# Kernel optimization log

Hardware: AMD Instinct MI355X
Metric: run time of the kernel (lower is better)

The kernel has to match this reference:

```python
import jax, jax.numpy as jnp
import numpy as np

N_ENTITIES = 100000
N_EDGES = 600000
N_RELATIONS = 24
D = 128


def setup_inputs() -> dict:
    key = jax.random.key(0)
    k1, k2, k3, k4 = jax.random.split(key, 4)
    ego_embed = jax.random.normal(k1, (N_ENTITIES, D), dtype=jnp.float32)
    edge_index = jax.random.randint(k2, (2, N_EDGES), 0, N_ENTITIES, dtype=jnp.int64)
    edge_type = jax.random.randint(k3, (N_EDGES,), 0, N_RELATIONS, dtype=jnp.int64)
    relation_weight = jax.random.normal(k4, (N_RELATIONS, D), dtype=jnp.float32)
    return {
        "ego_embed": ego_embed,
        "edge_index": edge_index,
        "edge_type": edge_type,
        "relation_weight": relation_weight,
    }


def reference(ego_embed, edge_index, edge_type, relation_weight):
    head, tail = edge_index[0], edge_index[1]
    n_entities = ego_embed.shape[0]
    # gather tail entity embeddings and relation embeddings, form messages
    msg = ego_embed[tail] * relation_weight[edge_type]  # [E, D]
    # scatter-mean aggregate messages per head entity
    agg = jax.ops.segment_sum(msg, head, num_segments=n_entities)  # [N, D]
    cnt = jax.ops.segment_sum(
        jnp.ones((msg.shape[0], 1), dtype=msg.dtype), head, num_segments=n_entities
    )  # [N, 1]
    entity_agg = agg / jnp.maximum(cnt, jnp.asarray(1, msg.dtype))
    return entity_agg
```

## Files before the change

kernel.cpp:

```cpp
#include <hip/hip_runtime.h>

#define D 128
#define CAP 32
#define SB 512
#define NREL 24
#define ABLOCKS 2048

__device__ __forceinline__ unsigned short f2bf_rne(float f) {
    unsigned b = __float_as_uint(f);
    b += 0x7fffu + ((b >> 16) & 1u);
    return (unsigned short)(b >> 16);
}


__global__ void conv_k(const float* __restrict__ in, ushort* __restrict__ outb, int n4,
                       int* __restrict__ cnt, int nEnt) {
    int g = blockIdx.x * blockDim.x + threadIdx.x;
    int stride = gridDim.x * blockDim.x;
    for (int j = g; j < nEnt; j += stride) cnt[j] = 0;
    const float4* __restrict__ in4 = (const float4*)in;
    ushort4* __restrict__ o4 = (ushort4*)outb;
    for (int i = g; i < n4; i += stride) {
        float4 v = in4[i];
        ushort4 o;
        o.x = f2bf_rne(v.x); o.y = f2bf_rne(v.y);
        o.z = f2bf_rne(v.z); o.w = f2bf_rne(v.w);
        o4[i] = o;
    }
}

__global__ void build_k(const int* __restrict__ head, const int* __restrict__ tail,
                        const int* __restrict__ etype, int* __restrict__ cnt,
                        unsigned* __restrict__ csr, int nE) {
    int i = blockIdx.x * blockDim.x + threadIdx.x;
    if (i < nE) {
        int h = head[i];
        int pos = atomicAdd(&cnt[h], 1);
        if (pos < CAP)
            csr[(size_t)h * CAP + pos] = ((unsigned)tail[i] << 5) | (unsigned)etype[i];
    }
}

__global__ void __launch_bounds__(256, 8)
agg6_k(const ushort* __restrict__ egob, const float* __restrict__ relw,
       const unsigned* __restrict__ csr, const int* __restrict__ cnt,
       float* __restrict__ out, int nEnt) {
    __shared__ float2 ldsw[32 * 64];

    int tid = threadIdx.x;
    const float2* __restrict__ rw2 = (const float2*)relw;
    for (int i = tid; i < NREL * 64; i += 256) ldsw[i] = rw2[i];
    __syncthreads();

    int gtid = blockIdx.x * 256 + tid;
    int w    = gtid >> 6;
    int lane = tid & 63;

    int nwaves = (ABLOCKS * 256) >> 6;
    int chunk  = (nEnt + nwaves - 1) / nwaves;
    int e0 = w * chunk;
    int e1 = e0 + chunk; if (e1 > nEnt) e1 = nEnt;

    const unsigned* __restrict__ eg = (const unsigned*)egob;
    float2* __restrict__ out2 = (float2*)out;

    for (int ent = e0; ent < e1; ++ent) {
        int c = __builtin_amdgcn_readfirstlane(cnt[ent]);
        int m = (c < CAP) ? c : CAP;
        const unsigned* __restrict__ row = csr + (size_t)ent * CAP;

        float ax = 0.f, ay = 0.f;

        for (int k = 0; k < m; k += 8) {
            uint4 q0 = *(const uint4*)(row + k);
            uint4 q1 = *(const uint4*)(row + k + 4);

            unsigned v0 = 0, v1 = 0, v2 = 0, v3 = 0, v4 = 0, v5 = 0, v6 = 0, v7 = 0;
            if (k + 0 < m) v0 = eg[(size_t)(q0.x >> 5) * 64 + lane];
            if (k + 1 < m) v1 = eg[(size_t)(q0.y >> 5) * 64 + lane];
            if (k + 2 < m) v2 = eg[(size_t)(q0.z >> 5) * 64 + lane];
            if (k + 3 < m) v3 = eg[(size_t)(q0.w >> 5) * 64 + lane];
            if (k + 4 < m) v4 = eg[(size_t)(q1.x >> 5) * 64 + lane];
            if (k + 5 < m) v5 = eg[(size_t)(q1.y >> 5) * 64 + lane];
            if (k + 6 < m) v6 = eg[(size_t)(q1.z >> 5) * 64 + lane];
            if (k + 7 < m) v7 = eg[(size_t)(q1.w >> 5) * 64 + lane];

            float2 w0 = ldsw[(q0.x & 31u) * 64 + lane];
            float2 w1 = ldsw[(q0.y & 31u) * 64 + lane];
            float2 w2 = ldsw[(q0.z & 31u) * 64 + lane];
            float2 w3 = ldsw[(q0.w & 31u) * 64 + lane];
            float2 w4 = ldsw[(q1.x & 31u) * 64 + lane];
            float2 w5 = ldsw[(q1.y & 31u) * 64 + lane];
            float2 w6 = ldsw[(q1.z & 31u) * 64 + lane];
            float2 w7 = ldsw[(q1.w & 31u) * 64 + lane];

            ax += __uint_as_float(v0 << 16) * w0.x; ay += __uint_as_float(v0 & 0xffff0000u) * w0.y;
            ax += __uint_as_float(v1 << 16) * w1.x; ay += __uint_as_float(v1 & 0xffff0000u) * w1.y;
            ax += __uint_as_float(v2 << 16) * w2.x; ay += __uint_as_float(v2 & 0xffff0000u) * w2.y;
            ax += __uint_as_float(v3 << 16) * w3.x; ay += __uint_as_float(v3 & 0xffff0000u) * w3.y;
            ax += __uint_as_float(v4 << 16) * w4.x; ay += __uint_as_float(v4 & 0xffff0000u) * w4.y;
            ax += __uint_as_float(v5 << 16) * w5.x; ay += __uint_as_float(v5 & 0xffff0000u) * w5.y;
            ax += __uint_as_float(v6 << 16) * w6.x; ay += __uint_as_float(v6 & 0xffff0000u) * w6.y;
            ax += __uint_as_float(v7 << 16) * w7.x; ay += __uint_as_float(v7 & 0xffff0000u) * w7.y;
        }

        float inv = 1.0f / fmaxf((float)c, 1.0f);
        float2 o; o.x = ax * inv; o.y = ay * inv;
        out2[(size_t)ent * 64 + lane] = o;
    }
}


__global__ void count_k(const int* __restrict__ head, int* __restrict__ counts, int nE) {
    int i = blockIdx.x * blockDim.x + threadIdx.x;
    if (i < nE) atomicAdd(&counts[head[i]], 1);
}

__global__ void blocksum_k(const int* __restrict__ counts, int* __restrict__ bsum, int nEnt) {
    __shared__ int s[SB];
    int t = threadIdx.x;
    int i = blockIdx.x * SB + t;
    s[t] = (i < nEnt) ? counts[i] : 0;
    __syncthreads();
    for (int off = SB / 2; off > 0; off >>= 1) {
        if (t < off) s[t] += s[t + off];
        __syncthreads();
    }
    if (t == 0) bsum[blockIdx.x] = s[0];
}

__global__ void scanb_k(int* __restrict__ bsum, int nSB) {
    __shared__ int s[SB];
    int t = threadIdx.x;
    int v = (t < nSB) ? bsum[t] : 0;
    s[t] = v;
    __syncthreads();
    for (int off = 1; off < SB; off <<= 1) {
        int x = (t >= off) ? s[t - off] : 0;
        __syncthreads();
        s[t] += x;
        __syncthreads();
    }
    if (t < nSB) bsum[t] = s[t] - v;
}

__global__ void writerows_k(const int* __restrict__ counts, const int* __restrict__ bsum,
                            int* __restrict__ rowstart, int* __restrict__ cursor, int nEnt) {
    __shared__ int s[SB];
    int t = threadIdx.x;
    int i = blockIdx.x * SB + t;
    int v = (i < nEnt) ? counts[i] : 0;
    s[t] = v;
    __syncthreads();
    for (int off = 1; off < SB; off <<= 1) {
        int x = (t >= off) ? s[t - off] : 0;
        __syncthreads();
        s[t] += x;
        __syncthreads();
    }
    if (i < nEnt) {
        int excl = s[t] - v + bsum[blockIdx.x];
        rowstart[i] = excl;
        cursor[i]   = excl;
    }
}

__global__ void bucket_k(const int* __restrict__ head, const int* __restrict__ tail,
                         const int* __restrict__ etype, int* __restrict__ cursor,
                         unsigned* __restrict__ csr, int nE) {
    int i = blockIdx.x * blockDim.x + threadIdx.x;
    if (i < nE) {
        int h = head[i];
        int pos = atomicAdd(&cursor[h], 1);
        csr[pos] = ((unsigned)tail[i] << 5) | (unsigned)etype[i];
    }
}

__global__ void agg_k(const float* __restrict__ ego, const float* __restrict__ relw,
                      const unsigned* __restrict__ csr, const int* __restrict__ rowstart,
                      const int* __restrict__ counts, float* __restrict__ out, int nEnt) {
    int gtid = blockIdx.x * blockDim.x + threadIdx.x;
    int wid  = gtid >> 6;
    int lane = gtid & 63;
    if (wid >= nEnt) return;
    int rs = __builtin_amdgcn_readfirstlane(rowstart[wid]);
    int c  = __builtin_amdgcn_readfirstlane(counts[wid]);
    const float2* __restrict__ ego2 = (const float2*)ego;
    const float2* __restrict__ rw2  = (const float2*)relw;
    float2 acc; acc.x = 0.f; acc.y = 0.f;
    unsigned u = (c > 0) ? csr[rs] : 0u;
    for (int k = 0; k < c; ++k) {
        unsigned un = (k + 1 < c) ? csr[rs + k + 1] : 0u;
        int t = (int)(u >> 5);
        int r = (int)(u & 31u);
        float2 v = ego2[(size_t)t * 64 + lane];
        float2 w = rw2[(size_t)r * 64 + lane];
        acc.x += v.x * w.x;
        acc.y += v.y * w.y;
        u = un;
    }
    float inv = 1.0f / fmaxf((float)c, 1.0f);
    float2 o; o.x = acc.x * inv; o.y = acc.y * inv;
    ((float2*)out)[(size_t)wid * 64 + lane] = o;
}

extern "C" void kernel_launch(void* const* d_in, const int* in_sizes, int n_in,
                              void* d_out, int out_size, void* d_ws, size_t ws_size,
                              hipStream_t stream) {
    const float* ego   = (const float*)d_in[0];
    const int*   eidx  = (const int*)d_in[1];
    const int*   etype = (const int*)d_in[2];
    const float* relw  = (const float*)d_in[3];
    float* out = (float*)d_out;

    int nE   = in_sizes[2];
    int nEnt = in_sizes[0] / D;
    const int* head = eidx;
    const int* tail = eidx + nE;

    char* ws = (char*)d_ws;
    size_t cntB  = (size_t)nEnt * 4;
    size_t csrB  = (size_t)nEnt * CAP * 4;
    size_t egoB  = (size_t)nEnt * D * 2;
    size_t needFast = cntB + csrB + egoB;

    int EB = (nE + 255) / 256;

    if (ws_size >= needFast) {
        int*      cnt  = (int*)ws;
        unsigned* csr  = (unsigned*)(ws + cntB);
        ushort*   egob = (ushort*)(ws + cntB + csrB);

        int n4 = nEnt * D / 4;
        conv_k<<<4096, 256, 0, stream>>>(ego, egob, n4, cnt, nEnt);
        build_k<<<EB, 256, 0, stream>>>(head, tail, etype, cnt, csr, nE);
        agg6_k<<<ABLOCKS, 256, 0, stream>>>(egob, relw, csr, cnt, out, nEnt);
    } else {
        int nSB = (nEnt + SB - 1) / SB;
        int*      counts   = (int*)ws;
        int*      rowstart = (int*)(ws + cntB);
        int*      cursor   = (int*)(ws + cntB * 2);
        int*      bsum     = (int*)(ws + cntB * 3);
        unsigned* csr      = (unsigned*)(ws + cntB * 3 + SB * 4);

        int ablocks = (int)(((size_t)nEnt * 64 + 255) / 256);
        hipMemsetAsync(counts, 0, cntB, stream);
        count_k<<<EB, 256, 0, stream>>>(head, counts, nE);
        blocksum_k<<<nSB, SB, 0, stream>>>(counts, bsum, nEnt);
        scanb_k<<<1, SB, 0, stream>>>(bsum, nSB);
        writerows_k<<<nSB, SB, 0, stream>>>(counts, bsum, rowstart, cursor, nEnt);
        bucket_k<<<EB, 256, 0, stream>>>(head, tail, etype, cursor, csr, nE);
        agg_k<<<ablocks, 256, 0, stream>>>(ego, relw, csr, rowstart, counts, out, nEnt);
    }
}
```

Measured before the change: 84.90 us.

## Split wave into four 16-lane groups each gathering a different edge with 16-byte loads

The aggregation kernel now assigns each 16-lane group of a wave its own edge, so every lane gathers 16 bytes (8 bf16 features) per edge with a uint4 load instead of 4 bytes. Per-lane accumulators cover 8 feature columns, and the four groups are combined with xor shuffles before group 0 writes the row as float4. The aim is fewer, wider memory transactions and fewer LDS reads per edge. In exchange it adds cross-lane reductions per entity, leaves lanes idle when an entity has few edges, and only one quarter of lanes do the stores.

Result: no change. 84.09 us (-1.0%).

```diff
diff --git a/kernel.cpp b/kernel.cpp
--- a/kernel.cpp
+++ b/kernel.cpp
@@ -42,71 +42,89 @@
 }
 
 __global__ void __launch_bounds__(256, 8)
-agg6_k(const ushort* __restrict__ egob, const float* __restrict__ relw,
+agg7_k(const ushort* __restrict__ egob, const float* __restrict__ relw,
        const unsigned* __restrict__ csr, const int* __restrict__ cnt,
        float* __restrict__ out, int nEnt) {
-    __shared__ float2 ldsw[32 * 64];
+    __shared__ float4 ldsw[32][32];
 
     int tid = threadIdx.x;
-    const float2* __restrict__ rw2 = (const float2*)relw;
-    for (int i = tid; i < NREL * 64; i += 256) ldsw[i] = rw2[i];
+    const float4* __restrict__ rw4 = (const float4*)relw;
+    for (int i = tid; i < NREL * 32; i += 256) ldsw[i >> 5][i & 31] = rw4[i];
     __syncthreads();
 
     int gtid = blockIdx.x * 256 + tid;
     int w    = gtid >> 6;
     int lane = tid & 63;
+    int grp  = lane >> 4;
+    int l16  = lane & 15;
 
     int nwaves = (ABLOCKS * 256) >> 6;
     int chunk  = (nEnt + nwaves - 1) / nwaves;
     int e0 = w * chunk;
     int e1 = e0 + chunk; if (e1 > nEnt) e1 = nEnt;
 
-    const unsigned* __restrict__ eg = (const unsigned*)egob;
-    float2* __restrict__ out2 = (float2*)out;
-
+    const uint4* __restrict__ eg16 = (const uint4*)egob;
+    
     for (int ent = e0; ent < e1; ++ent) {
         int c = __builtin_amdgcn_readfirstlane(cnt[ent]);
         int m = (c < CAP) ? c : CAP;
         const unsigned* __restrict__ row = csr + (size_t)ent * CAP;
 
-        float ax = 0.f, ay = 0.f;
+        float a0 = 0.f, a1 = 0.f, a2 = 0.f, a3 = 0.f;
+        float a4 = 0.f, a5 = 0.f, a6 = 0.f, a7 = 0.f;
 
         for (int k = 0; k < m; k += 8) {
-            uint4 q0 = *(const uint4*)(row + k);
-            uint4 q1 = *(const uint4*)(row + k + 4);
-
-            unsigned v0 = 0, v1 = 0, v2 = 0, v3 = 0, v4 = 0, v5 = 0, v6 = 0, v7 = 0;
-            if (k + 0 < m) v0 = eg[(size_t)(q0.x >> 5) * 64 + lane];
-            if (k + 1 < m) v1 = eg[(size_t)(q0.y >> 5) * 64 + lane];
-            if (k + 2 < m) v2 = eg[(size_t)(q0.z >> 5) * 64 + lane];
-            if (k + 3 < m) v3 = eg[(size_t)(q0.w >> 5) * 64 + lane];
-            if (k + 4 < m) v4 = eg[(size_t)(q1.x >> 5) * 64 + lane];
-            if (k + 5 < m) v5 = eg[(size_t)(q1.y >> 5) * 64 + lane];
-            if (k + 6 < m) v6 = eg[(size_t)(q1.z >> 5) * 64 + lane];
-            if (k + 7 < m) v7 = eg[(size_t)(q1.w >> 5) * 64 + lane];
-
-            float2 w0 = ldsw[(q0.x & 31u) * 64 + lane];
-            float2 w1 = ldsw[(q0.y & 31u) * 64 + lane];
-            float2 w2 = ldsw[(q0.z & 31u) * 64 + lane];
-            float2 w3 = ldsw[(q0.w & 31u) * 64 + lane];
-            float2 w4 = ldsw[(q1.x & 31u) * 64 + lane];
-            float2 w5 = ldsw[(q1.y & 31u) * 64 + lane];
-            float2 w6 = ldsw[(q1.z & 31u) * 64 + lane];
-            float2 w7 = ldsw[(q1.w & 31u) * 64 + lane];
-
-            ax += __uint_as_float(v0 << 16) * w0.x; ay += __uint_as_float(v0 & 0xffff0000u) * w0.y;
-            ax += __uint_as_float(v1 << 16) * w1.x; ay += __uint_as_float(v1 & 0xffff0000u) * w1.y;
-            ax += __uint_as_float(v2 << 16) * w2.x; ay += __uint_as_float(v2 & 0xffff0000u) * w2.y;
-            ax += __uint_as_float(v3 << 16) * w3.x; ay += __uint_as_float(v3 & 0xffff0000u) * w3.y;
-            ax += __uint_as_float(v4 << 16) * w4.x; ay += __uint_as_float(v4 & 0xffff0000u) * w4.y;
-            ax += __uint_as_float(v5 << 16) * w5.x; ay += __uint_as_float(v5 & 0xffff0000u) * w5.y;
-            ax += __uint_as_float(v6 << 16) * w6.x; ay += __uint_as_float(v6 & 0xffff0000u) * w6.y;
-            ax += __uint_as_float(v7 << 16) * w7.x; ay += __uint_as_float(v7 & 0xffff0000u) * w7.y;
+            bool pa = (k + grp) < m;
+            bool pb = (k + 4 + grp) < m;
+            unsigned ua = pa ? row[k + grp] : 0u;
+            unsigned ub = pb ? row[k + 4 + grp] : 0u;
+
+            uint4 va = make_uint4(0, 0, 0, 0);
+            uint4 vb = make_uint4(0, 0, 0, 0);
+            if (pa) va = eg16[(size_t)(ua >> 5) * 16 + l16];
+            if (pb) vb = eg16[(size_t)(ub >> 5) * 16 + l16];
+
+            float4 wa0 = ldsw[ua & 31u][l16 * 2];
+            float4 wa1 = ldsw[ua & 31u][l16 * 2 + 1];
+            float4 wb0 = ldsw[ub & 31u][l16 * 2];
+            float4 wb1 = ldsw[ub & 31u][l16 * 2 + 1];
+
+            a0 += __uint_as_float(va.x << 16)         * wa0.x;
+            a1 += __uint_as_float(va.x & 0xffff0000u) * wa0.y;
+            a2 += __uint_as_float(va.y << 16)         * wa0.z;
+            a3 += __uint_as_float(va.y & 0xffff0000u) * wa0.w;
+            a4 += __uint_as_float(va.z << 16)         * wa1.x;
+            a5 += __uint_as_float(va.z & 0xffff0000u) * wa1.y;
+            a6 += __uint_as_float(va.w << 16)         * wa1.z;
+            a7 += __uint_as_float(va.w & 0xffff0000u) * wa1.w;
+
+            a0 += __uint_as_float(vb.x << 16)         * wb0.x;
+            a1 += __uint_as_float(vb.x & 0xffff0000u) * wb0.y;
+            a2 += __uint_as_float(vb.y << 16)         * wb0.z;
+            a3 += __uint_as_float(vb.y & 0xffff0000u) * wb0.w;
+            a4 += __uint_as_float(vb.z << 16)         * wb1.x;
+            a5 += __uint_as_float(vb.z & 0xffff0000u) * wb1.y;
+            a6 += __uint_as_float(vb.w << 16)         * wb1.z;
+            a7 += __uint_as_float(vb.w & 0xffff0000u) * wb1.w;
         }
 
-        float inv = 1.0f / fmaxf((float)c, 1.0f);
-        float2 o; o.x = ax * inv; o.y = ay * inv;
-        out2[(size_t)ent * 64 + lane] = o;
+        a0 += __shfl_xor(a0, 16); a0 += __shfl_xor(a0, 32);
+        a1 += __shfl_xor(a1, 16); a1 += __shfl_xor(a1, 32);
+        a2 += __shfl_xor(a2, 16); a2 += __shfl_xor(a2, 32);
+        a3 += __shfl_xor(a3, 16); a3 += __shfl_xor(a3, 32);
+        a4 += __shfl_xor(a4, 16); a4 += __shfl_xor(a4, 32);
+        a5 += __shfl_xor(a5, 16); a5 += __shfl_xor(a5, 32);
+        a6 += __shfl_xor(a6, 16); a6 += __shfl_xor(a6, 32);
+        a7 += __shfl_xor(a7, 16); a7 += __shfl_xor(a7, 32);
+
+        if (grp == 0) {
+            float inv = 1.0f / fmaxf((float)c, 1.0f);
+            float4* __restrict__ orow = (float4*)(out + (size_t)ent * D);
+            float4 o0; o0.x = a0 * inv; o0.y = a1 * inv; o0.z = a2 * inv; o0.w = a3 * inv;
+            float4 o1; o1.x = a4 * inv; o1.y = a5 * inv; o1.z = a6 * inv; o1.w = a7 * inv;
+            orow[l16 * 2]     = o0;
+            orow[l16 * 2 + 1] = o1;
+        }
     }
 }
 
@@ -234,7 +252,7 @@
         int n4 = nEnt * D / 4;
         conv_k<<<4096, 256, 0, stream>>>(ego, egob, n4, cnt, nEnt);
         build_k<<<EB, 256, 0, stream>>>(head, tail, etype, cnt, csr, nE);
-        agg6_k<<<ABLOCKS, 256, 0, stream>>>(egob, relw, csr, cnt, out, nEnt);
+        agg7_k<<<ABLOCKS, 256, 0, stream>>>(egob, relw, csr, cnt, out, nEnt);
     } else {
         int nSB = (nEnt + SB - 1) / SB;
         int*      counts   = (int*)ws;
```
